# Kernel optimization log

Hardware: AMD Instinct MI355X
Metric: run time of the kernel (lower is better)

## Reference

```python
import jax, jax.numpy as jnp
import numpy as np

D, H, M, FF = 1024, 16, 64, 4096
B, N, C = 8, 1024, 256


def setup_inputs() -> dict:
    key = jax.random.key(0)
    it = iter(jax.random.split(key, 24))
    def nrm(shape, s):
        return jax.random.normal(next(it), shape, dtype=jnp.float32) * s
    z = lambda *s: jnp.zeros(s, jnp.float32)
    inp = {
        'point_tokens': nrm((B, N, D), 1.0),
        'context_tokens': nrm((B, C, D), 1.0),
        'inducing': nrm((1, M, D), 0.02),
    }
    for p in ('ti', 'tp'):  # to_induced / to_points MHA
        for w in ('Wq', 'Wk', 'Wv', 'Wo'):
            inp[f'{p}_{w}'] = nrm((D, D), 0.02)
        for b in ('bq', 'bk', 'bv', 'bo'):
            inp[f'{p}_{b}'] = z(D)
    for p in ('iff', 'pff'):  # induced_ff / point_ff: LN + Linear + GELU + Linear
        inp[f'{p}_g'] = jnp.ones(D, jnp.float32); inp[f'{p}_b'] = z(D)
        inp[f'{p}_W1'] = nrm((D, FF), 0.02); inp[f'{p}_b1'] = z(FF)
        inp[f'{p}_W2'] = nrm((FF, D), 0.02); inp[f'{p}_b2'] = z(D)
    inp['ni_g'] = jnp.ones(D, jnp.float32); inp['ni_b'] = z(D)
    inp['np_g'] = jnp.ones(D, jnp.float32); inp['np_b'] = z(D)
    return inp


def layernorm(x, g, b, eps=1e-5):
    mu = x.mean(-1, keepdims=True)
    var = ((x - mu) ** 2).mean(-1, keepdims=True)
    return (x - mu) * jax.lax.rsqrt(var + eps) * g + b


def ffn(x, g, b0, W1, b1, W2, b2):
    h = layernorm(x, g, b0)
    h = jax.nn.gelu(h @ W1 + b1, approximate=False)  # torch nn.GELU default = exact erf
    return h @ W2 + b2


def mha(q, kv, Wq, bq, Wk, bk, Wv, bv, Wo, bo):
    # torch nn.MultiheadAttention semantics (batch_first, dropout=0, need_weights=True)
    Bq, Lq, Dm = q.shape
    Lk = kv.shape[1]
    hd = Dm // H
    Q = (q @ Wq + bq).reshape(Bq, Lq, H, hd)
    K = (kv @ Wk + bk).reshape(Bq, Lk, H, hd)
    V = (kv @ Wv + bv).reshape(Bq, Lk, H, hd)
    scores = jnp.einsum('bqhd,bkhd->bhqk', Q, K) / jnp.sqrt(jnp.float32(hd))
    probs = jax.nn.softmax(scores, axis=-1)
    out = jnp.einsum('bhqk,bkhd->bqhd', probs, V).reshape(Bq, Lq, Dm)
    return out @ Wo + bo, probs.mean(axis=1)  # head-averaged weights (need_weights default)


def reference(point_tokens, context_tokens, inducing,
              ti_Wq, ti_bq, ti_Wk, ti_bk, ti_Wv, ti_bv, ti_Wo, ti_bo,
              tp_Wq, tp_bq, tp_Wk, tp_bk, tp_Wv, tp_bv, tp_Wo, tp_bo,
              iff_g, iff_b, iff_W1, iff_b1, iff_W2, iff_b2,
              pff_g, pff_b, pff_W1, pff_b1, pff_W2, pff_b2,
              ni_g, ni_b, np_g, np_b):
    b = point_tokens.shape[0]
    induced = jnp.broadcast_to(inducing, (b, inducing.shape[1], inducing.shape[2]))
    kv = jnp.concatenate([context_tokens, point_tokens], axis=1)
    ia, _ = mha(induced, kv, ti_Wq, ti_bq, ti_Wk, ti_bk, ti_Wv, ti_bv, ti_Wo, ti_bo)
    induced = layernorm(induced + ia, ni_g, ni_b)
    induced = induced + ffn(induced, iff_g, iff_b, iff_W1, iff_b1, iff_W2, iff_b2)
    kv2 = jnp.concatenate([context_tokens, induced], axis=1)
    pa, w2 = mha(point_tokens, kv2, tp_Wq, tp_bq, tp_Wk, tp_bk, tp_Wv, tp_bv, tp_Wo, tp_bo)
    pts = layernorm(point_tokens + pa, np_g, np_b)
    pts = pts + ffn(pts, pff_g, pff_b, pff_W1, pff_b1, pff_W2, pff_b2)
    probs = jnp.clip(w2, 1e-8, None)
    entropy = (-(probs * jnp.log(probs)).sum(axis=-1)).mean()  # detached side output
    return pts, entropy
```

## Files before the change

### kernel.cpp

```cpp
#include <hip/hip_runtime.h>
#include <hip/hip_bf16.h>
#include <math.h>

typedef unsigned short ushort_t;
typedef __attribute__((ext_vector_type(8))) short short8;
typedef __attribute__((ext_vector_type(4))) float f32x4;

static __device__ __forceinline__ ushort_t f2b(float f){
  union{float f;unsigned u;}a; a.f=f;
  unsigned r = a.u + 0x7fffu + ((a.u>>16)&1u);
  return (ushort_t)(r>>16);
}
static __device__ __forceinline__ float b2f(ushort_t u){
  union{unsigned u;float f;}a; a.u=((unsigned)u)<<16; return a.f;
}

#define GLDS16(g,l) __builtin_amdgcn_global_load_lds((const __attribute__((address_space(1))) void*)(const void*)(g), (__attribute__((address_space(3))) void*)(void*)(l), 16, 0, 0)

template<bool GELU, int RES>
__global__ __launch_bounds__(512, 2)
void gemm256q(const ushort_t* __restrict__ A, const ushort_t* __restrict__ Bt,
              const float* __restrict__ bias, const void* __restrict__ Res,
              float* __restrict__ Cf, ushort_t* __restrict__ Cb,
              int M, int N, int K, int lda, int ldb, int ldres, int ldcf, int ldcb,
              int nb0,
              long sA0, long sA1, long sB0, long sB1, long sR0, long sR1,
              long sCf0, long sCf1, long sCb0, long sCb1, float scale)
{
  const int z = blockIdx.z;
  const int zb0 = z % nb0, zb1 = z / nb0;
  A  += zb0*sA0 + zb1*sA1;
  Bt += zb0*sB0 + zb1*sB1;
  const float* RpF = 0; const ushort_t* RpB = 0;
  if (RES==1) RpF = (const float*)Res + zb0*sR0 + zb1*sR1;
  if (RES==2) RpB = (const ushort_t*)Res + zb0*sR0 + zb1*sR1;
  if (Cf) Cf += zb0*sCf0 + zb1*sCf1;
  if (Cb) Cb += zb0*sCb0 + zb1*sCb1;

  const int gx = gridDim.x;
  const int nwg = gx * gridDim.y;
  const int orig = blockIdx.y*gx + blockIdx.x;
  const int q8 = nwg >> 3, r8 = nwg & 7;
  const int xcd = orig & 7, ii = orig >> 3;
  const int wg = (xcd < r8 ? xcd*(q8+1) : r8*(q8+1) + (xcd-r8)*q8) + ii;
  const int bm = (wg / gx)*256, bn = (wg % gx)*256;

  __shared__ __align__(16) char As[2][32768];
  __shared__ __align__(16) char Bs[2][32768];

  const int tid = threadIdx.x, lane = tid&63, w = tid>>6;
  const int wr = w>>2, wc = w&3;
  const int lr = lane&15, g = lane>>4;
  const int e7 = lr & 7;

  f32x4 acc[8][4] = {};

  const int colElem = ((lane&7) ^ ((lane>>3)&7)) << 3;
  const int srRow = w*8 + (lane>>3);
  const ushort_t* pAst[4];
  const ushort_t* pBst[4];
#pragma unroll
  for (int a=0;a<4;a++){
    long r = min((long)(bm + a*64 + srRow), (long)M-1);
    pAst[a] = A + r*lda + colElem;
  }
#pragma unroll
  for (int b=0;b<4;b++){
    long r = min((long)(bn + b*64 + srRow), (long)N-1);
    pBst[b] = Bt + r*ldb + colElem;
  }

  const int NT = K >> 6;

#define STG256(Ad, Bd, ktEl) do { \
    GLDS16(pAst[0] + (ktEl), (Ad) + 0*8192 + w*1024); \
    GLDS16(pAst[1] + (ktEl), (Ad) + 1*8192 + w*1024); \
    GLDS16(pAst[2] + (ktEl), (Ad) + 2*8192 + w*1024); \
    GLDS16(pAst[3] + (ktEl), (Ad) + 3*8192 + w*1024); \
    GLDS16(pBst[0] + (ktEl), (Bd) + 0*8192 + w*1024); \
    GLDS16(pBst[1] + (ktEl), (Bd) + 1*8192 + w*1024); \
    GLDS16(pBst[2] + (ktEl), (Bd) + 2*8192 + w*1024); \
    GLDS16(pBst[3] + (ktEl), (Bd) + 3*8192 + w*1024); \
  } while(0)

  STG256(As[0], Bs[0], 0);
  __syncthreads();

  for (int t=0; t<NT; ++t){
    const char* Ab = As[t&1];
    const char* Bb = Bs[t&1];
    char* An = As[(t&1)^1];
    char* Bn = Bs[(t&1)^1];

    short8 bf[8];
#pragma unroll
    for (int n=0;n<4;n++)
#pragma unroll
      for (int s=0;s<2;s++)
        bf[n*2+s] = *(const short8*)(Bb + (wc*64 + n*16 + lr)*128 + (((g + 4*s) ^ e7) << 4));

    if (t+1 < NT) STG256(An, Bn, (long)(t+1)<<6);

#pragma unroll
    for (int mq=0; mq<4; mq++){
      short8 af[4];
#pragma unroll
      for (int mm=0;mm<2;mm++)
#pragma unroll
        for (int s=0;s<2;s++)
          af[mm*2+s] = *(const short8*)(Ab + (wr*128 + (mq*2+mm)*16 + lr)*128 + (((g + 4*s) ^ e7) << 4));
#pragma unroll
      for (int mm=0;mm<2;mm++)
#pragma unroll
        for (int n=0;n<4;n++)
#pragma unroll
        for (int s=0;s<2;s++)
          acc[mq*2+mm][n] = __builtin_amdgcn_mfma_f32_16x16x32_bf16(af[mm*2+s], bf[n*2+s], acc[mq*2+mm][n],0,0,0);
    }
    __syncthreads();
  }
#undef STG256

  const int orow = bm + wr*128, ocol = bn + wc*64;
  const int rsub = g*4;
#pragma unroll
  for (int n=0;n<4;n++){
    const int col = ocol + n*16 + lr;
    if (col >= N) continue;
    const float bv = bias ? bias[col] : 0.f;
#pragma unroll
    for (int m=0;m<8;m++){
#pragma unroll
      for (int i=0;i<4;i++){
        const int row = orow + m*16 + rsub + i;
        if (row >= M) continue;
        float v = acc[m][n][i]*scale + bv;
        if (GELU) v = 0.5f*v*(1.f + erff(v*0.70710678118654752f));
        if (RES==1) v += RpF[(long)row*ldres + col];
        if (RES==2) v += b2f(RpB[(long)row*ldres + col]);
        if (Cf) Cf[(long)row*ldcf + col] = v;
        if (Cb) Cb[(long)row*ldcb + col] = f2b(v);
      }
    }
  }
}

template<bool GELU, int RES>
__global__ __launch_bounds__(256)
void gemm_bt(const ushort_t* __restrict__ A, const ushort_t* __restrict__ Bt,
             const float* __restrict__ bias, const void* __restrict__ Res,
             float* __restrict__ Cf, ushort_t* __restrict__ Cb,
             int M, int N, int K, int lda, int ldb, int ldres, int ldcf, int ldcb,
             int nb0,
             long sA0, long sA1, long sB0, long sB1, long sR0, long sR1,
             long sCf0, long sCf1, long sCb0, long sCb1, float scale, int resMask)
{
  const int z = blockIdx.z;
  const int b0 = z % nb0, b1 = z / nb0;
  A  += b0*sA0 + b1*sA1;
  Bt += b0*sB0 + b1*sB1;
  const float* RpF = 0; const ushort_t* RpB = 0;
  if (RES==1) RpF = (const float*)Res + b0*sR0 + b1*sR1;
  if (RES==2) RpB = (const ushort_t*)Res + b0*sR0 + b1*sR1;
  if (Cf) Cf += b0*sCf0 + b1*sCf1;
  if (Cb) Cb += b0*sCb0 + b1*sCb1;

  const int gx = gridDim.x;
  const int nwg = gx * gridDim.y;
  const int orig = blockIdx.y*gx + blockIdx.x;
  const int q8 = nwg >> 3, r8 = nwg & 7;
  const int xcd = orig & 7, ii = orig >> 3;
  const int wg = (xcd < r8 ? xcd*(q8+1) : r8*(q8+1) + (xcd-r8)*q8) + ii;
  const int bm = (wg / gx)*128, bn = (wg % gx)*128;

  __shared__ __align__(16) ushort_t As[2][4096];
  __shared__ __align__(16) ushort_t Bs[2][4096];
  const int tid = threadIdx.x, lane = tid&63, wave = tid>>6;
  const int wr = wave>>1, wc = wave&1;

  f32x4 acc[4][4] = {};

  const int c0 = wave*64 + lane;
  const int c1 = c0 + 256;
  const long rA0 = min(bm + (c0>>2), M-1);
  const long rA1 = min(bm + (c1>>2), M-1);
  const long rB0 = min(bn + (c0>>2), N-1);
  const long rB1 = min(bn + (c1>>2), N-1);
  const ushort_t* pA0 = A + rA0*lda + (c0&3)*8;
  const ushort_t* pA1 = A + rA1*lda + (c1&3)*8;
  const ushort_t* pB0 = Bt + rB0*ldb + (c0&3)*8;
  const ushort_t* pB1 = Bt + rB1*ldb + (c1&3)*8;
  const int ldsOff = wave*512;

  const int lr = lane&15, lk = (lane>>4)*8;

#define STAGE(buf, kt) do { \
    GLDS16(pA0 + (kt), &As[buf][ldsOff]); \
    GLDS16(pA1 + (kt), &As[buf][2048 + ldsOff]); \
    GLDS16(pB0 + (kt), &Bs[buf][ldsOff]); \
    GLDS16(pB1 + (kt), &Bs[buf][2048 + ldsOff]); \
  } while(0)

  STAGE(0, 0);
  __syncthreads();
  int cur = 0;
  for (int kt = 0; kt < K; kt += 32) {
    if (kt + 32 < K) STAGE(cur^1, kt+32);
    short8 af[4], bfv[4];
#pragma unroll
    for (int m=0;m<4;m++) af[m]  = *(const short8*)(&As[cur][(wr*64+m*16+lr)*32 + lk]);
#pragma unroll
    for (int n=0;n<4;n++) bfv[n] = *(const short8*)(&Bs[cur][(wc*64+n*16+lr)*32 + lk]);
#pragma unroll
    for (int m=0;m<4;m++)
#pragma unroll
      for (int n=0;n<4;n++)
        acc[m][n] = __builtin_amdgcn_mfma_f32_16x16x32_bf16(af[m], bfv[n], acc[m][n], 0, 0, 0);
    __syncthreads();
    cur ^= 1;
  }
#undef STAGE

  const int orow = bm + wr*64, ocol = bn + wc*64;
  const int rsub = (lane>>4)*4;
#pragma unroll
  for (int n=0;n<4;n++){
    const int col = ocol + n*16 + lr;
    if (col >= N) continue;
    const float bv = bias ? bias[col] : 0.f;
#pragma unroll
    for (int m=0;m<4;m++){
#pragma unroll
      for (int i=0;i<4;i++){
        const int row = orow + m*16 + rsub + i;
        if (row >= M) continue;
        float v = acc[m][n][i]*scale + bv;
        if (GELU) v = 0.5f*v*(1.f + erff(v*0.70710678118654752f));
        if (RES==1) v += RpF[(long)(row & resMask)*ldres + col];
        if (RES==2) v += b2f(RpB[(long)(row & resMask)*ldres + col]);
        if (Cf) Cf[(long)row*ldcf + col] = v;
        if (Cb) Cb[(long)row*ldcb + col] = f2b(v);
      }
    }
  }
}

template<bool WRITEP>
__global__ __launch_bounds__(256)
void fattn_k(const ushort_t* __restrict__ Qb, const ushort_t* __restrict__ KVb,
             const ushort_t* __restrict__ Vtb, ushort_t* __restrict__ Ob,
             ushort_t* __restrict__ Pb,
             int LK, int ldkv, int qRowsPerB, int oRowsPerB, float scale)
{
  const int z = blockIdx.z, b = z >> 4, h = z & 15;
  const int qt = blockIdx.x;
  const int tid = threadIdx.x, lane = tid & 63, wave = tid >> 6;
  const int lr = lane & 15, g = lane >> 4;

  __shared__ __align__(16) ushort_t Kls[64*68];
  __shared__ __align__(16) ushort_t Vtls[64*68];
  __shared__ __align__(16) ushort_t Pls[64*68];

  const long qrow = (long)b*qRowsPerB + qt*64 + wave*16 + lr;
  const short8 aq0 = *(const short8*)(Qb + qrow*1024 + h*64 + g*8);
  const short8 aq1 = *(const short8*)(Qb + qrow*1024 + h*64 + 32 + g*8);

  const ushort_t* Kbase = KVb + (long)b*LK*ldkv + h*64;
  const ushort_t* Vtbase = Vtb + (long)(b*16+h)*64*LK;

  const int ntiles = LK >> 6;
  const int r0 = tid>>3, d0c = (tid&7)*8;
  const int r1 = r0 + 32;

  float m[4] = {-3e30f,-3e30f,-3e30f,-3e30f};
  float l[4] = {0.f,0.f,0.f,0.f};

  for (int t=0; t<ntiles; ++t){
    __syncthreads();
    { short8 v0 = *(const short8*)(Kbase + (long)(t*64 + r0)*ldkv + d0c);
      short8 v1 = *(const short8*)(Kbase + (long)(t*64 + r1)*ldkv + d0c);
      *(short8*)(Kls + r0*68 + d0c) = v0;
      *(short8*)(Kls + r1*68 + d0c) = v1; }
    __syncthreads();
    f32x4 s[4];
#pragma unroll
    for(int n=0;n<4;n++){
      s[n] = (f32x4){0.f,0.f,0.f,0.f};
      short8 bk0 = *(const short8*)(Kls + (n*16+lr)*68 + g*8);
      short8 bk1 = *(const short8*)(Kls + (n*16+lr)*68 + 32 + g*8);
      s[n] = __builtin_amdgcn_mfma_f32_16x16x32_bf16(aq0, bk0, s[n],0,0,0);
      s[n] = __builtin_amdgcn_mfma_f32_16x16x32_bf16(aq1, bk1, s[n],0,0,0);
    }
#pragma unroll
    for(int i=0;i<4;i++){
      float mx = fmaxf(fmaxf(s[0][i],s[1][i]), fmaxf(s[2][i],s[3][i])) * scale;
#pragma unroll
      for(int o2=1;o2<16;o2<<=1) mx = fmaxf(mx, __shfl_xor(mx,o2));
      float mnew = fmaxf(m[i], mx);
      float sum = __expf(s[0][i]*scale-mnew)+__expf(s[1][i]*scale-mnew)
                + __expf(s[2][i]*scale-mnew)+__expf(s[3][i]*scale-mnew);
#pragma unroll
      for(int o2=1;o2<16;o2<<=1) sum += __shfl_xor(sum,o2);
      l[i] = l[i]*__expf(m[i]-mnew) + sum;
      m[i] = mnew;
    }
  }
  float invl[4];
#pragma unroll
  for(int i=0;i<4;i++) invl[i] = 1.f/l[i];

  f32x4 o[4];
#pragma unroll
  for(int n=0;n<4;n++) o[n] = (f32x4){0.f,0.f,0.f,0.f};

  long pbase = 0;
  if (WRITEP) pbase = ((long)(b*16+h)*1024 + qt*64 + wave*16)*320 + lr;

  for (int t=0; t<ntiles; ++t){
    __syncthreads();
    { short8 v0 = *(const short8*)(Kbase + (long)(t*64 + r0)*ldkv + d0c);
      short8 v1 = *(const short8*)(Kbase + (long)(t*64 + r1)*ldkv + d0c);
      short8 w0 = *(const short8*)(Vtbase + (long)r0*LK + t*64 + d0c);
      short8 w1 = *(const short8*)(Vtbase + (long)r1*LK + t*64 + d0c);
      *(short8*)(Kls + r0*68 + d0c) = v0;
      *(short8*)(Kls + r1*68 + d0c) = v1;
      *(short8*)(Vtls + r0*68 + d0c) = w0;
      *(short8*)(Vtls + r1*68 + d0c) = w1; }
    __syncthreads();
    f32x4 s[4];
#pragma unroll
    for(int n=0;n<4;n++){
      s[n] = (f32x4){0.f,0.f,0.f,0.f};
      short8 bk0 = *(const short8*)(Kls + (n*16+lr)*68 + g*8);
      short8 bk1 = *(const short8*)(Kls + (n*16+lr)*68 + 32 + g*8);
      s[n] = __builtin_amdgcn_mfma_f32_16x16x32_bf16(aq0, bk0, s[n],0,0,0);
      s[n] = __builtin_amdgcn_mfma_f32_16x16x32_bf16(aq1, bk1, s[n],0,0,0);
    }
#pragma unroll
    for(int n=0;n<4;n++){
#pragma unroll
      for(int i=0;i<4;i++){
        float e = __expf(s[n][i]*scale - m[i]);
        Pls[(wave*16 + g*4 + i)*68 + n*16 + lr] = f2b(e);
        if (WRITEP) Pb[pbase + (long)(g*4+i)*320 + t*64 + n*16] = f2b(e*invl[i]);
      }
    }
    short8 pa0 = *(const short8*)(Pls + (wave*16+lr)*68 + g*8);
    short8 pa1 = *(const short8*)(Pls + (wave*16+lr)*68 + 32 + g*8);
#pragma unroll
    for(int nd=0; nd<4; nd++){
      short8 vb0 = *(const short8*)(Vtls + (nd*16+lr)*68 + g*8);
      short8 vb1 = *(const short8*)(Vtls + (nd*16+lr)*68 + 32 + g*8);
      o[nd] = __builtin_amdgcn_mfma_f32_16x16x32_bf16(pa0, vb0, o[nd],0,0,0);
      o[nd] = __builtin_amdgcn_mfma_f32_16x16x32_bf16(pa1, vb1, o[nd],0,0,0);
    }
  }
  const long orow0 = (long)b*oRowsPerB + qt*64 + wave*16 + g*4;
#pragma unroll
  for(int nd=0;nd<4;nd++)
#pragma unroll
    for(int i=0;i<4;i++)
      Ob[(orow0+i)*1024 + h*64 + nd*16 + lr] = f2b(o[nd][i]*invl[i]);
}

__global__ __launch_bounds__(256)
void tcvt_k(const float* __restrict__ src, ushort_t* __restrict__ dst, int R, int C)
{
  __shared__ float t[32][33];
  int c0 = blockIdx.x*32, r0 = blockIdx.y*32;
  int tx = threadIdx.x & 31, ty = threadIdx.x >> 5;
  for (int i=ty;i<32;i+=8){ int r=r0+i, c=c0+tx; t[i][tx] = (r<R && c<C) ? src[(long)r*C + c] : 0.f; }
  __syncthreads();
  for (int i=ty;i<32;i+=8){ int c=c0+i, r=r0+tx; if (c<C && r<R) dst[(long)c*R + r] = f2b(t[tx][i]); }
}

__global__ __launch_bounds__(256)
void cvt_rows_k(const float* __restrict__ src, ushort_t* __restrict__ dst,
                long total, int R, long dstBS, long dstRO)
{
  long e = ((long)blockIdx.x*256 + threadIdx.x)*4;
  if (e >= total) return;
  long rc = e >> 10; int c = (int)(e & 1023);
  int r = (int)(rc % R); long b = rc / R;
  float4 v = *(const float4*)(src + e);
  ushort4 o; o.x=f2b(v.x); o.y=f2b(v.y); o.z=f2b(v.z); o.w=f2b(v.w);
  *(ushort4*)(dst + (b*dstBS + dstRO + r)*1024 + c) = o;
}

__global__ __launch_bounds__(256)
void vtrans_k(const ushort_t* __restrict__ V, ushort_t* __restrict__ Vt,
              int Lk, int ldv, int coloff)
{
  int b = blockIdx.z, h = blockIdx.y, k0 = blockIdx.x*32;
  __shared__ ushort_t t[32][65];
  int tx = threadIdx.x & 63, ty = threadIdx.x >> 6;
  for (int i=ty;i<32;i+=4) t[i][tx] = V[((long)b*Lk + k0 + i)*ldv + coloff + h*64 + tx];
  __syncthreads();
  int kk = threadIdx.x & 31, n0 = threadIdx.x >> 5;
  for (int n=n0;n<64;n+=8) Vt[((long)(b*16+h)*64 + n)*Lk + k0 + kk] = t[kk][n];
}

__global__ __launch_bounds__(256)
void ln2x_k(const float* __restrict__ x,
            const float* __restrict__ g1, const float* __restrict__ b1,
            const float* __restrict__ g2, const float* __restrict__ b2,
            float* __restrict__ y1f, ushort_t* __restrict__ y1b, ushort_t* __restrict__ y2b)
{
  const long row = blockIdx.x;
  int tid = threadIdx.x, lane = tid&63, wave = tid>>6;
  __shared__ float red[8], red2[8];
  float4 v = ((const float4*)(x + row*1024))[tid];
  float s = v.x+v.y+v.z+v.w;
  for (int o=32;o;o>>=1) s += __shfl_down(s,o);
  if (lane==0) red[wave]=s;
  __syncthreads();
  float mean = (red[0]+red[1]+red[2]+red[3])*(1.f/1024.f);
  float d0=v.x-mean, d1=v.y-mean, d2=v.z-mean, d3=v.w-mean;
  float q = d0*d0+d1*d1+d2*d2+d3*d3;
  for (int o=32;o;o>>=1) q += __shfl_down(q,o);
  if (lane==0) red[4+wave]=q;
  __syncthreads();
  float var = (red[4]+red[5]+red[6]+red[7])*(1.f/1024.f);
  float rs = rsqrtf(var+1e-5f);
  float4 gg=((const float4*)g1)[tid], bb=((const float4*)b1)[tid];
  float y0=d0*rs*gg.x+bb.x, y1v=d1*rs*gg.y+bb.y, y2v=d2*rs*gg.z+bb.z, y3=d3*rs*gg.w+bb.w;
  if (y1f) ((float4*)(y1f+row*1024))[tid] = make_float4(y0,y1v,y2v,y3);
  if (y1b){ ushort4 o4; o4.x=f2b(y0); o4.y=f2b(y1v); o4.z=f2b(y2v); o4.w=f2b(y3);
            ((ushort4*)(y1b+row*1024))[tid]=o4; }
  float s2 = y0+y1v+y2v+y3;
  for (int o=32;o;o>>=1) s2 += __shfl_down(s2,o);
  if (lane==0) red2[wave]=s2;
  __syncthreads();
  float mean2 = (red2[0]+red2[1]+red2[2]+red2[3])*(1.f/1024.f);
  float e0=y0-mean2,e1=y1v-mean2,e2=y2v-mean2,e3=y3-mean2;
  float q2 = e0*e0+e1*e1+e2*e2+e3*e3;
  for (int o=32;o;o>>=1) q2 += __shfl_down(q2,o);
  if (lane==0) red2[4+wave]=q2;
  __syncthreads();
  float var2 = (red2[4]+red2[5]+red2[6]+red2[7])*(1.f/1024.f);
  float rs2 = rsqrtf(var2+1e-5f);
  float4 g2v=((const float4*)g2)[tid], b2v=((const float4*)b2)[tid];
  ushort4 o4;
  o4.x=f2b(e0*rs2*g2v.x+b2v.x); o4.y=f2b(e1*rs2*g2v.y+b2v.y);
  o4.z=f2b(e2*rs2*g2v.z+b2v.z); o4.w=f2b(e3*rs2*g2v.w+b2v.w);
  ((ushort4*)(y2b+row*1024))[tid]=o4;
}

__global__ __launch_bounds__(256)
void w2ent_k(const ushort_t* __restrict__ P, float* __restrict__ rowent)
{
  int wid = (int)((blockIdx.x*256 + threadIdx.x) >> 6);
  int lane = threadIdx.x & 63;
  int b = wid >> 10, q = wid & 1023;
  const ushort_t* base = P + ((long)(b*16)*1024 + q)*320;
  float acc = 0.f;
#pragma unroll
  for (int j=0;j<5;j++){
    int k = j*64 + lane;
    float s = 0.f;
#pragma unroll
    for (int h=0;h<16;h++) s += b2f(base[(long)h*327680 + k]);
    float p = fmaxf(s*(1.f/16.f), 1e-8f);
    acc += p*__logf(p);
  }
  for (int o=32;o;o>>=1) acc += __shfl_down(acc, o);
  if (lane==0) rowent[wid] = acc;
}

__global__ __launch_bounds__(256)
void entfin_k(const float* __restrict__ rowent, float* __restrict__ out)
{
  float s = 0.f;
  for (int i=threadIdx.x;i<8192;i+=256) s += rowent[i];
  __shared__ float red[4];
  for (int o=32;o;o>>=1) s += __shfl_down(s,o);
  if ((threadIdx.x&63)==0) red[threadIdx.x>>6]=s;
  __syncthreads();
  if (threadIdx.x==0) out[0] = -(red[0]+red[1]+red[2]+red[3]) * (1.f/8192.f);
}

__global__ void dbg_k(float* out, float a){ out[0] = -12345.f; out[1] = a; }

static void gemm(hipStream_t s, int mode,
                 const void* A, const void* Bt, const float* bias, const void* Res,
                 void* Cf, void* Cb,
                 int M, int N, int K, int lda, int ldb, int ldres, int ldcf, int ldcb,
                 int nz, int nb0,
                 long sA0, long sA1, long sB0, long sB1, long sR0, long sR1,
                 long sCf0, long sCf1, long sCb0, long sCb1, float scale, int resMask)
{
  dim3 g((N+127)/128, (M+127)/128, nz), b(256,1,1);
#define ARGS (const ushort_t*)A,(const ushort_t*)Bt,bias,Res,(float*)Cf,(ushort_t*)Cb,M,N,K,lda,ldb,ldres,ldcf,ldcb,nb0,sA0,sA1,sB0,sB1,sR0,sR1,sCf0,sCf1,sCb0,sCb1,scale,resMask
  if      (mode == 1) gemm_bt<true ,0><<<g,b,0,s>>>(ARGS);
  else if (mode == 2) gemm_bt<false,1><<<g,b,0,s>>>(ARGS);
  else if (mode == 3) gemm_bt<false,2><<<g,b,0,s>>>(ARGS);
  else                gemm_bt<false,0><<<g,b,0,s>>>(ARGS);
#undef ARGS
}

static void g256(hipStream_t s, int mode,
                 const void* A, const void* Bt, const float* bias, const void* Res,
                 void* Cf, void* Cb,
                 int M, int N, int K, int lda, int ldb, int ldres, int ldcf, int ldcb,
                 int nz, int nb0,
                 long sA0, long sA1, long sB0, long sB1, long sR0, long sR1,
                 long sCf0, long sCf1, long sCb0, long sCb1, float scale)
{
  dim3 g((N+255)/256, (M+255)/256, nz), b(512,1,1);
#define ARGS (const ushort_t*)A,(const ushort_t*)Bt,bias,Res,(float*)Cf,(ushort_t*)Cb,M,N,K,lda,ldb,ldres,ldcf,ldcb,nb0,sA0,sA1,sB0,sB1,sR0,sR1,sCf0,sCf1,sCb0,sCb1,scale
  if      (mode == 1) gemm256q<true ,0><<<g,b,0,s>>>(ARGS);
  else if (mode == 2) gemm256q<false,1><<<g,b,0,s>>>(ARGS);
  else if (mode == 3) gemm256q<false,2><<<g,b,0,s>>>(ARGS);
  else                gemm256q<false,0><<<g,b,0,s>>>(ARGS);
#undef ARGS
}

extern "C" void kernel_launch(void* const* d_in, const int* in_sizes, int n_in,
                              void* d_out, int out_size, void* d_ws, size_t ws_size,
                              hipStream_t stream)
{
  const float* ptsIn = (const float*)d_in[0];
  const float* ctx   = (const float*)d_in[1];
  const float* induc = (const float*)d_in[2];
  const float* tiW[4]={(const float*)d_in[3],(const float*)d_in[4],(const float*)d_in[5],(const float*)d_in[6]};
  const float* tib[4]={(const float*)d_in[7],(const float*)d_in[8],(const float*)d_in[9],(const float*)d_in[10]};
  const float* tpW[4]={(const float*)d_in[11],(const float*)d_in[12],(const float*)d_in[13],(const float*)d_in[14]};
  const float* tpb[4]={(const float*)d_in[15],(const float*)d_in[16],(const float*)d_in[17],(const float*)d_in[18]};
  const float* iff_g=(const float*)d_in[19]; const float* iff_b=(const float*)d_in[20];
  const float* iffW1=(const float*)d_in[21]; const float* iff_b1=(const float*)d_in[22];
  const float* iffW2=(const float*)d_in[23]; const float* iff_b2=(const float*)d_in[24];
  const float* pff_g=(const float*)d_in[25]; const float* pff_b=(const float*)d_in[26];
  const float* pffW1=(const float*)d_in[27]; const float* pff_b1=(const float*)d_in[28];
  const float* pffW2=(const float*)d_in[29]; const float* pff_b2=(const float*)d_in[30];
  const float* ni_g=(const float*)d_in[31]; const float* ni_b=(const float*)d_in[32];
  const float* np_g=(const float*)d_in[33]; const float* np_b=(const float*)d_in[34];
  float* outF = (float*)d_out;

  char* ws = (char*)d_ws;
  size_t off = 0;
  auto alloc = [&](size_t bytes){ off=(off+255)&~(size_t)255; size_t o=off; off+=bytes; return o; };
  auto sub = [&](size_t& pp, size_t bytes){ pp=(pp+255)&~(size_t)255; size_t o=pp; pp+=bytes; return o; };

  size_t o_tiQw  = alloc(1024L*1024*2);
  size_t o_tiKVw = alloc(2048L*1024*2);
  size_t o_tiOw  = alloc(1024L*1024*2);
  size_t o_tpQw  = alloc(1024L*1024*2);
  size_t o_tpKVw = alloc(2048L*1024*2);
  size_t o_tpOw  = alloc(1024L*1024*2);
  size_t o_iffW1t = alloc(4096L*1024*2);
  size_t o_iffW2t = alloc(4096L*1024*2);
  size_t o_pffW1t = alloc(4096L*1024*2);
  size_t o_pffW2t = alloc(4096L*1024*2);
  size_t o_bti  = alloc(2048*4);
  size_t o_btp  = alloc(2048*4);
  size_t o_indb = alloc(64L*1024*2);
  size_t o_kv   = alloc(10240L*1024*2);
  size_t o_kv2  = alloc(2560L*1024*2);
  size_t o_rowent = alloc(8192*4);
  off=(off+255)&~(size_t)255;
  size_t arena = off;

  size_t p = arena;
  size_t o_Qti     = sub(p, 64L*1024*2);
  size_t o_KVti    = sub(p, 10240L*2048*2);
  size_t o_Vtti    = sub(p, 8192L*1280*2);
  size_t o_attnOti = sub(p, 512L*1024*2);
  size_t o_t1      = sub(p, 512L*1024*4);
  size_t o_ind1    = sub(p, 512L*1024*4);
  size_t o_h0i     = sub(p, 512L*1024*2);
  size_t o_h1i     = sub(p, 512L*4096*2);
  size_t need1 = p;
  p = arena;
  size_t o_attnOtp = sub(p, 8192L*1024*2);
  size_t shared = p;
  size_t o_Qtp  = sub(p, 8192L*1024*2);
  size_t o_KVtp = sub(p, 2560L*2048*2);
  size_t o_Vttp = sub(p, 8192L*320*2);
  size_t o_P    = sub(p, 8L*16*1024*320*2);
  size_t need3 = p;
  p = shared;
  size_t o_t2   = sub(p, 8192L*1024*4);
  size_t o_pts1 = sub(p, 8192L*1024*2);
  size_t o_h0p  = sub(p, 8192L*1024*2);
  size_t o_h1p  = sub(p, 8192L*4096*2);
  size_t need4 = p;

  size_t need = need1;
  if (need3>need) need=need3;
  if (need4>need) need=need4;
  if (need > ws_size){ dbg_k<<<1,1,0,stream>>>(outF, (float)(need>>20)); return; }

#define WP(o) ((void*)(ws + (o)))
#define BP(o) ((ushort_t*)(ws + (o)))
#define FP(o) ((float*)(ws + (o)))

  tcvt_k<<<dim3(32,32),256,0,stream>>>(tiW[0], BP(o_tiQw), 1024, 1024);
  tcvt_k<<<dim3(32,32),256,0,stream>>>(tiW[1], BP(o_tiKVw), 1024, 1024);
  tcvt_k<<<dim3(32,32),256,0,stream>>>(tiW[2], BP(o_tiKVw) + 1024L*1024, 1024, 1024);
  tcvt_k<<<dim3(32,32),256,0,stream>>>(tiW[3], BP(o_tiOw), 1024, 1024);
  tcvt_k<<<dim3(32,32),256,0,stream>>>(tpW[0], BP(o_tpQw), 1024, 1024);
  tcvt_k<<<dim3(32,32),256,0,stream>>>(tpW[1], BP(o_tpKVw), 1024, 1024);
  tcvt_k<<<dim3(32,32),256,0,stream>>>(tpW[2], BP(o_tpKVw) + 1024L*1024, 1024, 1024);
  tcvt_k<<<dim3(32,32),256,0,stream>>>(tpW[3], BP(o_tpOw), 1024, 1024);
  tcvt_k<<<dim3(128,32),256,0,stream>>>(iffW1, BP(o_iffW1t), 1024, 4096);
  tcvt_k<<<dim3(32,128),256,0,stream>>>(iffW2, BP(o_iffW2t), 4096, 1024);
  tcvt_k<<<dim3(128,32),256,0,stream>>>(pffW1, BP(o_pffW1t), 1024, 4096);
  tcvt_k<<<dim3(32,128),256,0,stream>>>(pffW2, BP(o_pffW2t), 4096, 1024);
  hipMemcpyAsync(WP(o_bti), (const void*)tib[1], 1024*4, hipMemcpyDeviceToDevice, stream);
  hipMemcpyAsync((void*)(ws+o_bti+1024*4), (const void*)tib[2], 1024*4, hipMemcpyDeviceToDevice, stream);
  hipMemcpyAsync(WP(o_btp), (const void*)tpb[1], 1024*4, hipMemcpyDeviceToDevice, stream);
  hipMemcpyAsync((void*)(ws+o_btp+1024*4), (const void*)tpb[2], 1024*4, hipMemcpyDeviceToDevice, stream);

  cvt_rows_k<<<2048,256,0,stream>>>(ctx,   BP(o_kv),  8L*256*1024, 256, 1280, 0);
  cvt_rows_k<<<8192,256,0,stream>>>(ptsIn, BP(o_kv),  8L*1024*1024, 1024, 1280, 256);
  cvt_rows_k<<<64,256,0,stream>>>(induc,   BP(o_indb), 64L*1024, 64, 64, 0);
  cvt_rows_k<<<2048,256,0,stream>>>(ctx,   BP(o_kv2), 8L*256*1024, 256, 320, 0);

  gemm(stream,0, WP(o_indb), WP(o_tiQw), tib[0], 0, 0, WP(o_Qti),
       64,1024,1024, 1024,1024,0,0,1024, 1,1, 0,0,0,0,0,0,0,0,0,0, 1.f,-1);
  g256(stream,0, WP(o_kv), WP(o_tiKVw), FP(o_bti), 0, 0, WP(o_KVti),
       10240,2048,1024, 1024,1024,0,0,2048, 1,1, 0,0,0,0,0,0,0,0,0,0, 1.f);
  vtrans_k<<<dim3(40,16,8),256,0,stream>>>(BP(o_KVti), BP(o_Vtti), 1280, 2048, 1024);
  fattn_k<false><<<dim3(1,1,128),256,0,stream>>>(BP(o_Qti), BP(o_KVti), BP(o_Vtti),
       BP(o_attnOti), (ushort_t*)0, 1280, 2048, 0, 64, 0.125f);
  gemm(stream,2, WP(o_attnOti), WP(o_tiOw), tib[3], (const void*)induc, WP(o_t1), 0,
       512,1024,1024, 1024,1024,1024,1024,0, 1,1, 0,0,0,0,0,0,0,0,0,0, 1.f,63);
  ln2x_k<<<512,256,0,stream>>>(FP(o_t1), ni_g, ni_b, iff_g, iff_b, FP(o_ind1), 0, BP(o_h0i));
  gemm(stream,1, WP(o_h0i), WP(o_iffW1t), iff_b1, 0, 0, WP(o_h1i),
       512,4096,1024, 1024,1024,0,0,4096, 1,1, 0,0,0,0,0,0,0,0,0,0, 1.f,-1);
  gemm(stream,2, WP(o_h1i), WP(o_iffW2t), iff_b2, WP(o_ind1), 0, BP(o_kv2) + 262144,
       64,1024,4096, 4096,4096,1024,0,1024, 8,8,
       262144,0, 0,0, 65536,0, 0,0, 327680,0, 1.f,-1);

  g256(stream,0, BP(o_kv) + 262144, WP(o_tpQw), tpb[0], 0, 0, WP(o_Qtp),
       1024,1024,1024, 1024,1024,0,0,1024, 8,8,
       1310720,0, 0,0, 0,0, 0,0, 1048576,0, 1.f);
  g256(stream,0, WP(o_kv2), WP(o_tpKVw), FP(o_btp), 0, 0, WP(o_KVtp),
       2560,2048,1024, 1024,1024,0,0,2048, 1,1, 0,0,0,0,0,0,0,0,0,0, 1.f);
  vtrans_k<<<dim3(10,16,8),256,0,stream>>>(BP(o_KVtp), BP(o_Vttp), 320, 2048, 1024);
  fattn_k<true><<<dim3(16,1,128),256,0,stream>>>(BP(o_Qtp), BP(o_KVtp), BP(o_Vttp),
       BP(o_attnOtp), BP(o_P), 320, 2048, 1024, 1024, 0.125f);
  w2ent_k<<<2048,256,0,stream>>>(BP(o_P), FP(o_rowent));
  entfin_k<<<1,256,0,stream>>>(FP(o_rowent), outF + (out_size-1));
  g256(stream,2, WP(o_attnOtp), WP(o_tpOw), tpb[3], (const void*)ptsIn, WP(o_t2), 0,
       8192,1024,1024, 1024,1024,1024,1024,0, 1,1, 0,0,0,0,0,0,0,0,0,0, 1.f);
  ln2x_k<<<8192,256,0,stream>>>(FP(o_t2), np_g, np_b, pff_g, pff_b, 0, BP(o_pts1), BP(o_h0p));
  g256(stream,1, WP(o_h0p), WP(o_pffW1t), pff_b1, 0, 0, WP(o_h1p),
       8192,4096,1024, 1024,1024,0,0,4096, 1,1, 0,0,0,0,0,0,0,0,0,0, 1.f);
  g256(stream,3, WP(o_h1p), WP(o_pffW2t), pff_b2, WP(o_pts1), outF, 0,
       8192,1024,4096, 4096,4096,1024,1024,0, 1,1, 0,0,0,0,0,0,0,0,0,0, 1.f);

#undef WP
#undef BP
#undef FP
}
```

Measured before the change: 0.9999 ms.

## Rewrite 256x256 GEMM main loop as 4-stage K=32 LDS pipeline with setprio

The large-tile bf16 GEMM kernel now splits each K=64 step into four K=32 LDS stages in a ring buffer. Global-to-LDS loads run up to three stages ahead, controlled by explicit vmcnt waits and a single barrier per stage. MFMA blocks are wrapped in s_setprio to favour math issue, and the LDS swizzle is changed to match the 64-byte rows. The smaller KV projection for the second attention moves back to the 128-tile gemm, presumably to fill more CUs. The risks are that a single barrier per stage may race with the stage being overwritten, and that per-stage loads are smaller.

```diff
diff --git a/kernel.cpp b/kernel.cpp
--- a/kernel.cpp
+++ b/kernel.cpp
@@ -19,13 +19,13 @@
 
 template<bool GELU, int RES>
 __global__ __launch_bounds__(512, 2)
-void gemm256q(const ushort_t* __restrict__ A, const ushort_t* __restrict__ Bt,
-              const float* __restrict__ bias, const void* __restrict__ Res,
-              float* __restrict__ Cf, ushort_t* __restrict__ Cb,
-              int M, int N, int K, int lda, int ldb, int ldres, int ldcf, int ldcb,
-              int nb0,
-              long sA0, long sA1, long sB0, long sB1, long sR0, long sR1,
-              long sCf0, long sCf1, long sCb0, long sCb1, float scale)
+void gemm8p(const ushort_t* __restrict__ A, const ushort_t* __restrict__ Bt,
+            const float* __restrict__ bias, const void* __restrict__ Res,
+            float* __restrict__ Cf, ushort_t* __restrict__ Cb,
+            int M, int N, int K, int lda, int ldb, int ldres, int ldcf, int ldcb,
+            int nb0,
+            long sA0, long sA1, long sB0, long sB1, long sR0, long sR1,
+            long sCf0, long sCf1, long sCb0, long sCb1, float scale)
 {
   const int z = blockIdx.z;
   const int zb0 = z % nb0, zb1 = z / nb0;
@@ -45,81 +45,71 @@
   const int wg = (xcd < r8 ? xcd*(q8+1) : r8*(q8+1) + (xcd-r8)*q8) + ii;
   const int bm = (wg / gx)*256, bn = (wg % gx)*256;
 
-  __shared__ __align__(16) char As[2][32768];
-  __shared__ __align__(16) char Bs[2][32768];
+  __shared__ __align__(16) char As[4][16384];
+  __shared__ __align__(16) char Bs[4][16384];
 
   const int tid = threadIdx.x, lane = tid&63, w = tid>>6;
   const int wr = w>>2, wc = w&3;
   const int lr = lane&15, g = lane>>4;
-  const int e7 = lr & 7;
+  const int fld = ((g ^ (lr&3)) << 4);
 
   f32x4 acc[8][4] = {};
 
-  const int colElem = ((lane&7) ^ ((lane>>3)&7)) << 3;
-  const int srRow = w*8 + (lane>>3);
-  const ushort_t* pAst[4];
-  const ushort_t* pBst[4];
-#pragma unroll
-  for (int a=0;a<4;a++){
-    long r = min((long)(bm + a*64 + srRow), (long)M-1);
-    pAst[a] = A + r*lda + colElem;
-  }
-#pragma unroll
-  for (int b=0;b<4;b++){
-    long r = min((long)(bn + b*64 + srRow), (long)N-1);
-    pBst[b] = Bt + r*ldb + colElem;
-  }
-
-  const int NT = K >> 6;
-
-#define STG256(Ad, Bd, ktEl) do { \
-    GLDS16(pAst[0] + (ktEl), (Ad) + 0*8192 + w*1024); \
-    GLDS16(pAst[1] + (ktEl), (Ad) + 1*8192 + w*1024); \
-    GLDS16(pAst[2] + (ktEl), (Ad) + 2*8192 + w*1024); \
-    GLDS16(pAst[3] + (ktEl), (Ad) + 3*8192 + w*1024); \
-    GLDS16(pBst[0] + (ktEl), (Bd) + 0*8192 + w*1024); \
-    GLDS16(pBst[1] + (ktEl), (Bd) + 1*8192 + w*1024); \
-    GLDS16(pBst[2] + (ktEl), (Bd) + 2*8192 + w*1024); \
-    GLDS16(pBst[3] + (ktEl), (Bd) + 3*8192 + w*1024); \
+  const int colElem = (((lane&3) ^ ((lane>>2)&3)) << 3);
+  const int srRow = w*16 + (lane>>2);
+  const ushort_t* pA[2]; const ushort_t* pB[2];
+#pragma unroll
+  for (int j=0;j<2;j++){
+    long rA = min((long)(bm + j*128 + srRow), (long)M-1);
+    long rB = min((long)(bn + j*128 + srRow), (long)N-1);
+    pA[j] = A + rA*lda + colElem;
+    pB[j] = Bt + rB*ldb + colElem;
+  }
+
+  const int NT = K >> 6, NU = NT >> 1;
+
+#define STG8(IDX, elemOff) do { \
+    GLDS16(pA[0] + (elemOff), As[IDX] + w*1024); \
+    GLDS16(pA[1] + (elemOff), As[IDX] + 8192 + w*1024); \
+    GLDS16(pB[0] + (elemOff), Bs[IDX] + w*1024); \
+    GLDS16(pB[1] + (elemOff), Bs[IDX] + 8192 + w*1024); \
   } while(0)
 
-  STG256(As[0], Bs[0], 0);
-  __syncthreads();
-
-  for (int t=0; t<NT; ++t){
-    const char* Ab = As[t&1];
-    const char* Bb = Bs[t&1];
-    char* An = As[(t&1)^1];
-    char* Bn = Bs[(t&1)^1];
-
-    short8 bf[8];
-#pragma unroll
-    for (int n=0;n<4;n++)
-#pragma unroll
-      for (int s=0;s<2;s++)
-        bf[n*2+s] = *(const short8*)(Bb + (wc*64 + n*16 + lr)*128 + (((g + 4*s) ^ e7) << 4));
-
-    if (t+1 < NT) STG256(An, Bn, (long)(t+1)<<6);
-
-#pragma unroll
-    for (int mq=0; mq<4; mq++){
-      short8 af[4];
-#pragma unroll
-      for (int mm=0;mm<2;mm++)
-#pragma unroll
-        for (int s=0;s<2;s++)
-          af[mm*2+s] = *(const short8*)(Ab + (wr*128 + (mq*2+mm)*16 + lr)*128 + (((g + 4*s) ^ e7) << 4));
-#pragma unroll
-      for (int mm=0;mm<2;mm++)
-#pragma unroll
-        for (int n=0;n<4;n++)
-#pragma unroll
-        for (int s=0;s<2;s++)
-          acc[mq*2+mm][n] = __builtin_amdgcn_mfma_f32_16x16x32_bf16(af[mm*2+s], bf[n*2+s], acc[mq*2+mm][n],0,0,0);
-    }
-    __syncthreads();
-  }
-#undef STG256
+  STG8(0, 0);
+  STG8(1, 32);
+  STG8(2, 64);
+  asm volatile("s_waitcnt vmcnt(8)" ::: "memory");
+  __builtin_amdgcn_s_barrier();
+  asm volatile("" ::: "memory");
+
+  for (int u=0; u<NU; ++u){
+    const long tb = (long)u*128;
+    const bool st = (u+1 < NU);
+#pragma unroll
+    for (int ph=0; ph<4; ++ph){
+      const int RD = ph;
+      const int SW = (ph+3)&3;
+      const long se = tb + 96 + ph*32;
+      const bool dost = (ph==0) ? true : st;
+      asm volatile("s_waitcnt vmcnt(4)" ::: "memory");
+      short8 a_[8]; short8 b_[4];
+#pragma unroll
+      for (int m_=0;m_<8;m_++) a_[m_] = *(const short8*)(As[RD] + (wr*128 + m_*16 + lr)*64 + fld);
+#pragma unroll
+      for (int n_=0;n_<4;n_++) b_[n_] = *(const short8*)(Bs[RD] + (wc*64 + n_*16 + lr)*64 + fld);
+      if (dost) STG8(SW, se);
+      __builtin_amdgcn_s_barrier();
+      asm volatile("" ::: "memory");
+      __builtin_amdgcn_s_setprio(1);
+#pragma unroll
+      for (int m_=0;m_<8;m_++)
+#pragma unroll
+        for (int n_=0;n_<4;n_++)
+          acc[m_][n_] = __builtin_amdgcn_mfma_f32_16x16x32_bf16(a_[m_], b_[n_], acc[m_][n_],0,0,0);
+      __builtin_amdgcn_s_setprio(0);
+    }
+  }
+#undef STG8
 
   const int orow = bm + wr*128, ocol = bn + wc*64;
   const int rsub = g*4;
@@ -498,20 +488,20 @@
 #undef ARGS
 }
 
-static void g256(hipStream_t s, int mode,
-                 const void* A, const void* Bt, const float* bias, const void* Res,
-                 void* Cf, void* Cb,
-                 int M, int N, int K, int lda, int ldb, int ldres, int ldcf, int ldcb,
-                 int nz, int nb0,
-                 long sA0, long sA1, long sB0, long sB1, long sR0, long sR1,
-                 long sCf0, long sCf1, long sCb0, long sCb1, float scale)
+static void g8(hipStream_t s, int mode,
+               const void* A, const void* Bt, const float* bias, const void* Res,
+               void* Cf, void* Cb,
+               int M, int N, int K, int lda, int ldb, int ldres, int ldcf, int ldcb,
+               int nz, int nb0,
+               long sA0, long sA1, long sB0, long sB1, long sR0, long sR1,
+               long sCf0, long sCf1, long sCb0, long sCb1, float scale)
 {
   dim3 g((N+255)/256, (M+255)/256, nz), b(512,1,1);
 #define ARGS (const ushort_t*)A,(const ushort_t*)Bt,bias,Res,(float*)Cf,(ushort_t*)Cb,M,N,K,lda,ldb,ldres,ldcf,ldcb,nb0,sA0,sA1,sB0,sB1,sR0,sR1,sCf0,sCf1,sCb0,sCb1,scale
-  if      (mode == 1) gemm256q<true ,0><<<g,b,0,s>>>(ARGS);
-  else if (mode == 2) gemm256q<false,1><<<g,b,0,s>>>(ARGS);
-  else if (mode == 3) gemm256q<false,2><<<g,b,0,s>>>(ARGS);
-  else                gemm256q<false,0><<<g,b,0,s>>>(ARGS);
+  if      (mode == 1) gemm8p<true ,0><<<g,b,0,s>>>(ARGS);
+  else if (mode == 2) gemm8p<false,1><<<g,b,0,s>>>(ARGS);
+  else if (mode == 3) gemm8p<false,2><<<g,b,0,s>>>(ARGS);
+  else                gemm8p<false,0><<<g,b,0,s>>>(ARGS);
 #undef ARGS
 }
 
@@ -618,7 +608,7 @@
 
   gemm(stream,0, WP(o_indb), WP(o_tiQw), tib[0], 0, 0, WP(o_Qti),
        64,1024,1024, 1024,1024,0,0,1024, 1,1, 0,0,0,0,0,0,0,0,0,0, 1.f,-1);
-  g256(stream,0, WP(o_kv), WP(o_tiKVw), FP(o_bti), 0, 0, WP(o_KVti),
+  g8(stream,0, WP(o_kv), WP(o_tiKVw), FP(o_bti), 0, 0, WP(o_KVti),
        10240,2048,1024, 1024,1024,0,0,2048, 1,1, 0,0,0,0,0,0,0,0,0,0, 1.f);
   vtrans_k<<<dim3(40,16,8),256,0,stream>>>(BP(o_KVti), BP(o_Vtti), 1280, 2048, 1024);
   fattn_k<false><<<dim3(1,1,128),256,0,stream>>>(BP(o_Qti), BP(o_KVti), BP(o_Vtti),
@@ -632,22 +622,22 @@
        64,1024,4096, 4096,4096,1024,0,1024, 8,8,
        262144,0, 0,0, 65536,0, 0,0, 327680,0, 1.f,-1);
 
-  g256(stream,0, BP(o_kv) + 262144, WP(o_tpQw), tpb[0], 0, 0, WP(o_Qtp),
+  g8(stream,0, BP(o_kv) + 262144, WP(o_tpQw), tpb[0], 0, 0, WP(o_Qtp),
        1024,1024,1024, 1024,1024,0,0,1024, 8,8,
        1310720,0, 0,0, 0,0, 0,0, 1048576,0, 1.f);
-  g256(stream,0, WP(o_kv2), WP(o_tpKVw), FP(o_btp), 0, 0, WP(o_KVtp),
-       2560,2048,1024, 1024,1024,0,0,2048, 1,1, 0,0,0,0,0,0,0,0,0,0, 1.f);
+  gemm(stream,0, WP(o_kv2), WP(o_tpKVw), FP(o_btp), 0, 0, WP(o_KVtp),
+       2560,2048,1024, 1024,1024,0,0,2048, 1,1, 0,0,0,0,0,0,0,0,0,0, 1.f,-1);
   vtrans_k<<<dim3(10,16,8),256,0,stream>>>(BP(o_KVtp), BP(o_Vttp), 320, 2048, 1024);
   fattn_k<true><<<dim3(16,1,128),256,0,stream>>>(BP(o_Qtp), BP(o_KVtp), BP(o_Vttp),
        BP(o_attnOtp), BP(o_P), 320, 2048, 1024, 1024, 0.125f);
   w2ent_k<<<2048,256,0,stream>>>(BP(o_P), FP(o_rowent));
   entfin_k<<<1,256,0,stream>>>(FP(o_rowent), outF + (out_size-1));
-  g256(stream,2, WP(o_attnOtp), WP(o_tpOw), tpb[3], (const void*)ptsIn, WP(o_t2), 0,
+  g8(stream,2, WP(o_attnOtp), WP(o_tpOw), tpb[3], (const void*)ptsIn, WP(o_t2), 0,
        8192,1024,1024, 1024,1024,1024,1024,0, 1,1, 0,0,0,0,0,0,0,0,0,0, 1.f);
   ln2x_k<<<8192,256,0,stream>>>(FP(o_t2), np_g, np_b, pff_g, pff_b, 0, BP(o_pts1), BP(o_h0p));
-  g256(stream,1, WP(o_h0p), WP(o_pffW1t), pff_b1, 0, 0, WP(o_h1p),
+  g8(stream,1, WP(o_h0p), WP(o_pffW1t), pff_b1, 0, 0, WP(o_h1p),
        8192,4096,1024, 1024,1024,0,0,4096, 1,1, 0,0,0,0,0,0,0,0,0,0, 1.f);
-  g256(stream,3, WP(o_h1p), WP(o_pffW2t), pff_b2, WP(o_pts1), outF, 0,
+  g8(stream,3, WP(o_h1p), WP(o_pffW2t), pff_b2, WP(o_pts1), outF, 0,
        8192,1024,4096, 4096,4096,1024,1024,0, 1,1, 0,0,0,0,0,0,0,0,0,0, 1.f);
 
 #undef WP
```

New measurement: 1.028 ms. 2.8% more time.
